# Kernel optimization log

Hardware: AMD Instinct MI355X
Metric: run time of the kernel (lower is better)

Reference implementation:

```python
import jax, jax.numpy as jnp
import numpy as np

B, T, U = 4, 256, 100
H_ENC, H_DEC = 512, 512
INPUT_SIZE = H_ENC + H_DEC  # 1024, joint='concat'
INNER = 512
VOCAB = 1024


def setup_inputs() -> dict:
    key = jax.random.key(0)
    k1, k2, k3, k4, k5, k6 = jax.random.split(key, 6)
    s_in = 1.0 / np.sqrt(INPUT_SIZE)
    s_h = 1.0 / np.sqrt(INNER)
    return {
        "enc_state": jax.random.normal(k1, (B, T, H_ENC), dtype=jnp.float32),
        "dec_state": jax.random.normal(k2, (B, U, H_DEC), dtype=jnp.float32),
        # mlp[0]: Linear(input_size -> inner): W1 [inner, input_size], b1 [inner]
        "W1": jax.random.uniform(k3, (INNER, INPUT_SIZE), jnp.float32, -s_in, s_in),
        "b1": jax.random.uniform(k4, (INNER,), jnp.float32, -s_in, s_in),
        # mlp[2]: Linear(inner -> vocab): W2 [vocab, inner], b2 [vocab]
        "W2": jax.random.uniform(k5, (VOCAB, INNER), jnp.float32, -s_h, s_h),
        "b2": jax.random.uniform(k6, (VOCAB,), jnp.float32, -s_h, s_h),
    }


def reference(enc_state, dec_state, W1, b1, W2, b2):
    # joint='concat': concat([enc broadcast over U, dec broadcast over T], -1)
    # then Linear -> tanh -> Linear.
    # Mathematically identical fused form: split W1 into enc/dec column blocks,
    # project each at native size, broadcast-add.
    h_enc = H_ENC
    W1e = W1[:, :h_enc]   # [inner, H_enc]
    W1d = W1[:, h_enc:]   # [inner, H_dec]
    pe = jnp.einsum('bth,ih->bti', enc_state, W1e)  # [B,T,inner]
    pd = jnp.einsum('buh,ih->bui', dec_state, W1d)  # [B,U,inner]
    hidden = jnp.tanh(pe[:, :, None, :] + pd[:, None, :, :] + b1)  # [B,T,U,inner]
    joint = jnp.einsum('btui,vi->btuv', hidden, W2) + b2  # [B,T,U,vocab]
    return joint
```

## Files before the change

kernel.cpp:

```cpp
#include <hip/hip_runtime.h>
#include <hip/hip_bf16.h>

#define NB 4
#define NT 256
#define NU 100
#define NH 512
#define NI 512
#define NV 1024
#define MROWS (NB * NT * NU)

typedef __attribute__((ext_vector_type(4))) float f32x4;
typedef __attribute__((ext_vector_type(8))) __bf16 bf16x8;

static __device__ __forceinline__ unsigned int f2bf(float f) {
  unsigned int u = __float_as_uint(f);
  return (u + 0x7FFFu + ((u >> 16) & 1u)) >> 16;
}

static __device__ __forceinline__ float fast_tanh(float x) {
  float e = __expf(2.f * x);
  return 1.f - 2.f * __builtin_amdgcn_rcpf(1.f + e);
}

static __device__ __forceinline__ unsigned int cvt_pk_bf16(float lo, float hi) {
  unsigned int r;
  asm("v_cvt_pk_bf16_f32 %0, %1, %2" : "=v"(r) : "v"(lo), "v"(hi));
  return r;
}

__global__ __launch_bounds__(256) void proj_kernel(
    const float* __restrict__ enc, const float* __restrict__ dec,
    const float* __restrict__ W1, float* __restrict__ pe, float* __restrict__ pd) {
  __shared__ float As[64][17];
  __shared__ float Bs[64][17];
  const int bx = blockIdx.x;
  const float* A;
  float* P;
  int Mrows, colOff, row0;
  if (bx < 16) { A = enc; P = pe; Mrows = NB * NT; colOff = 0;  row0 = bx * 64; }
  else         { A = dec; P = pd; Mrows = NB * NU; colOff = NH; row0 = (bx - 16) * 64; }
  const int col0 = blockIdx.y * 64;
  const int tx = threadIdx.x;
  const int tr = tx >> 4, tc = tx & 15;
  const int lr = tx >> 2, lc = (tx & 3) * 4;
  float acc[4][4] = {};
  for (int k0 = 0; k0 < NH; k0 += 16) {
    float4 av = make_float4(0.f, 0.f, 0.f, 0.f);
    if (row0 + lr < Mrows)
      av = *(const float4*)(A + (size_t)(row0 + lr) * NH + k0 + lc);
    float4 bv = *(const float4*)(W1 + (size_t)(col0 + lr) * (NH + NH) + colOff + k0 + lc);
    As[lr][lc] = av.x; As[lr][lc + 1] = av.y; As[lr][lc + 2] = av.z; As[lr][lc + 3] = av.w;
    Bs[lr][lc] = bv.x; Bs[lr][lc + 1] = bv.y; Bs[lr][lc + 2] = bv.z; Bs[lr][lc + 3] = bv.w;
    __syncthreads();
#pragma unroll
    for (int kk = 0; kk < 16; ++kk) {
      float a4[4], b4[4];
#pragma unroll
      for (int i = 0; i < 4; ++i) { a4[i] = As[tr * 4 + i][kk]; b4[i] = Bs[tc * 4 + i][kk]; }
#pragma unroll
      for (int i = 0; i < 4; ++i)
#pragma unroll
        for (int j = 0; j < 4; ++j) acc[i][j] = fmaf(a4[i], b4[j], acc[i][j]);
    }
    __syncthreads();
  }
#pragma unroll
  for (int i = 0; i < 4; ++i) {
    int r = row0 + tr * 4 + i;
    if (r < Mrows) {
#pragma unroll
      for (int j = 0; j < 4; ++j)
        P[(size_t)r * NI + col0 + tc * 4 + j] = acc[i][j];
    }
  }
}

__global__ __launch_bounds__(256) void cvt_w2_frag_kernel(
    const float* __restrict__ W2, unsigned short* __restrict__ w2f) {
  int g = blockIdx.x * 256 + threadIdx.x;
  int lr = g & 15, lq = (g >> 4) & 3;
  int cb = (g >> 6) & 15, kt = (g >> 10) & 15, nt = (g >> 14) & 3;
  int v = nt * 256 + cb * 16 + lr;
  int k = kt * 32 + lq * 8;
  const float* src = W2 + (size_t)v * NI + k;
  float4 a = *(const float4*)src;
  float4 b = *(const float4*)(src + 4);
  uint4 o;
  o.x = f2bf(a.x) | (f2bf(a.y) << 16);
  o.y = f2bf(a.z) | (f2bf(a.w) << 16);
  o.z = f2bf(b.x) | (f2bf(b.y) << 16);
  o.w = f2bf(b.z) | (f2bf(b.w) << 16);
  *(uint4*)(w2f + (size_t)g * 8) = o;
}

__global__ __launch_bounds__(512, 2) void fused_joint_kernel(
    const float* __restrict__ pe, const float* __restrict__ pd,
    const float* __restrict__ b1, const unsigned short* __restrict__ w2f,
    const float* __restrict__ b2, float* __restrict__ out) {
  __shared__ unsigned char ldsA[131072];
  const int tx = threadIdx.x;
  const int R0 = blockIdx.x * 128;
  const int lane = tx & 63, wid = tx >> 6;
  const int wr = wid >> 2, wc = wid & 3;
  const int lr = lane & 15, lq = lane >> 4;

  const unsigned short* w2base = w2f + ((size_t)(wc * 4) * 64 + lq * 16 + lr) * 8;
#define LOADB(DST, G) do {                                                    \
    const unsigned short* s_ = w2base + ((size_t)(G) << 13);                  \
    DST##0 = *(const bf16x8*)(s_);                                            \
    DST##1 = *(const bf16x8*)(s_ + 512);                                      \
    DST##2 = *(const bf16x8*)(s_ + 1024);                                     \
    DST##3 = *(const bf16x8*)(s_ + 1536);                                     \
  } while (0)

  bf16x8 bA0, bA1, bA2, bA3, bB0, bB1, bB2, bB3;
  LOADB(bA, 0);

#pragma unroll 2
  for (int pass = 0; pass < 16; ++pass) {
    int idx = pass * 512 + tx;
    int row = idx >> 6;
    int g8 = idx & 63;
    int i0 = g8 * 8;
    int grow = R0 + row;
    int b = grow / (NT * NU);
    int rem = grow - b * (NT * NU);
    int t = rem / NU;
    int u = rem - t * NU;
    const float* peP = pe + (size_t)(b * NT + t) * NI + i0;
    const float* pdP = pd + (size_t)(b * NU + u) * NI + i0;
    float4 p0 = *(const float4*)peP, p1 = *(const float4*)(peP + 4);
    float4 q0 = *(const float4*)pdP, q1 = *(const float4*)(pdP + 4);
    float4 c0 = *(const float4*)(b1 + i0), c1 = *(const float4*)(b1 + i0 + 4);
    uint4 pk;
    pk.x = cvt_pk_bf16(fast_tanh(p0.x + q0.x + c0.x), fast_tanh(p0.y + q0.y + c0.y));
    pk.y = cvt_pk_bf16(fast_tanh(p0.z + q0.z + c0.z), fast_tanh(p0.w + q0.w + c0.w));
    pk.z = cvt_pk_bf16(fast_tanh(p1.x + q1.x + c1.x), fast_tanh(p1.y + q1.y + c1.y));
    pk.w = cvt_pk_bf16(fast_tanh(p1.z + q1.z + c1.z), fast_tanh(p1.w + q1.w + c1.w));
    *(uint4*)(ldsA + row * 1024 + ((g8 ^ (row & 7)) << 4)) = pk;
  }
  __syncthreads();

  f32x4 acc[4][4];
#pragma unroll
  for (int mf = 0; mf < 4; ++mf)
#pragma unroll
    for (int nf = 0; nf < 4; ++nf)
#pragma unroll
      for (int z = 0; z < 4; ++z) acc[mf][nf][z] = 0.f;

#define COMPUTE(BV, G) do {                                                   \
    const int kt_ = (G) & 15;                                                 \
    bf16x8 af_[4];                                                            \
    _Pragma("unroll")                                                         \
    for (int mf = 0; mf < 4; ++mf) {                                          \
      int row_ = wr * 64 + mf * 16 + lr;                                      \
      af_[mf] = *(const bf16x8*)(ldsA + row_ * 1024 +                         \
                                 (((kt_ * 4 + lq) ^ (lr & 7)) << 4));         \
    }                                                                         \
    __builtin_amdgcn_s_setprio(1);                                            \
    _Pragma("unroll")                                                         \
    for (int mf = 0; mf < 4; ++mf) {                                          \
      acc[mf][0] = __builtin_amdgcn_mfma_f32_16x16x32_bf16(af_[mf], BV##0, acc[mf][0], 0, 0, 0); \
      acc[mf][1] = __builtin_amdgcn_mfma_f32_16x16x32_bf16(af_[mf], BV##1, acc[mf][1], 0, 0, 0); \
      acc[mf][2] = __builtin_amdgcn_mfma_f32_16x16x32_bf16(af_[mf], BV##2, acc[mf][2], 0, 0, 0); \
      acc[mf][3] = __builtin_amdgcn_mfma_f32_16x16x32_bf16(af_[mf], BV##3, acc[mf][3], 0, 0, 0); \
    }                                                                         \
    __builtin_amdgcn_s_setprio(0);                                            \
    if (kt_ == 15) {                                                          \
      const int np_ = (G) >> 4;                                               \
      _Pragma("unroll")                                                       \
      for (int nf = 0; nf < 4; ++nf) {                                        \
        int col_ = np_ * 256 + wc * 64 + nf * 16 + lr;                        \
        float bb_ = b2[col_];                                                 \
        _Pragma("unroll")                                                     \
        for (int mf = 0; mf < 4; ++mf) {                                      \
          _Pragma("unroll")                                                   \
          for (int j = 0; j < 4; ++j) {                                       \
            int grow_ = R0 + wr * 64 + mf * 16 + lq * 4 + j;                  \
            out[(size_t)grow_ * NV + col_] = acc[mf][nf][j] + bb_;            \
            acc[mf][nf][j] = 0.f;                                             \
          }                                                                   \
        }                                                                     \
      }                                                                       \
    }                                                                         \
  } while (0)

  for (int g = 0; g < 64; g += 2) {
    LOADB(bB, g + 1);
    COMPUTE(bA, g);
    if (g + 2 < 64) LOADB(bA, g + 2);
    COMPUTE(bB, g + 1);
  }
#undef COMPUTE
#undef LOADB
}

extern "C" void kernel_launch(void* const* d_in, const int* in_sizes, int n_in,
                              void* d_out, int out_size, void* d_ws, size_t ws_size,
                              hipStream_t stream) {
  const float* enc = (const float*)d_in[0];
  const float* dec = (const float*)d_in[1];
  const float* W1  = (const float*)d_in[2];
  const float* b1  = (const float*)d_in[3];
  const float* W2  = (const float*)d_in[4];
  const float* b2  = (const float*)d_in[5];
  float* out = (float*)d_out;
  char* ws = (char*)d_ws;

  float* pe = (float*)ws;
  float* pd = (float*)(ws + (2u << 20));
  unsigned short* w2f = (unsigned short*)(ws + (3u << 20));

  proj_kernel<<<dim3(23, 8), 256, 0, stream>>>(enc, dec, W1, pe, pd);
  cvt_w2_frag_kernel<<<256, 256, 0, stream>>>(W2, w2f);
  fused_joint_kernel<<<MROWS / 128, 512, 0, stream>>>(pe, pd, b1, w2f, b2, out);
}
```

Before: 228.6 us.

## Stage W2 tiles into double-buffered LDS via global_load_lds

The W2 operand was loaded straight from global memory into registers by each wave. It is now copied cooperatively into a double-buffered 32KB LDS region using the asynchronous global-to-LDS load instruction. Each wave then reads its B fragments from LDS, so the waves that share a column group no longer fetch duplicate global data, and VGPR pressure from the prefetch registers goes down. In exchange the loop adds a block-wide barrier on every k-step and extra LDS reads, and the block's LDS footprint grows to 160KB.

```diff
diff --git a/kernel.cpp b/kernel.cpp
--- a/kernel.cpp
+++ b/kernel.cpp
@@ -26,6 +26,12 @@
   unsigned int r;
   asm("v_cvt_pk_bf16_f32 %0, %1, %2" : "=v"(r) : "v"(lo), "v"(hi));
   return r;
+}
+
+static __device__ __forceinline__ void gload16(const void* g, void* l) {
+  __builtin_amdgcn_global_load_lds(
+      (const __attribute__((address_space(1))) unsigned int*)(g),
+      (__attribute__((address_space(3))) unsigned int*)(l), 16, 0, 0);
 }
 
 __global__ __launch_bounds__(256) void proj_kernel(
@@ -98,23 +104,21 @@
     const float* __restrict__ b1, const unsigned short* __restrict__ w2f,
     const float* __restrict__ b2, float* __restrict__ out) {
   __shared__ unsigned char ldsA[131072];
+  __shared__ unsigned char ldsB[32768];
   const int tx = threadIdx.x;
   const int R0 = blockIdx.x * 128;
   const int lane = tx & 63, wid = tx >> 6;
   const int wr = wid >> 2, wc = wid & 3;
   const int lr = lane & 15, lq = lane >> 4;
 
-  const unsigned short* w2base = w2f + ((size_t)(wc * 4) * 64 + lq * 16 + lr) * 8;
-#define LOADB(DST, G) do {                                                    \
-    const unsigned short* s_ = w2base + ((size_t)(G) << 13);                  \
-    DST##0 = *(const bf16x8*)(s_);                                            \
-    DST##1 = *(const bf16x8*)(s_ + 512);                                      \
-    DST##2 = *(const bf16x8*)(s_ + 1024);                                     \
-    DST##3 = *(const bf16x8*)(s_ + 1536);                                     \
+#define STAGEB(G, SLOT) do {                                                  \
+    unsigned char* dB_ = ldsB + (SLOT) * 16384;                               \
+    const unsigned char* src_ = (const unsigned char*)w2f + ((size_t)(G) << 14); \
+    gload16(src_ + tx * 16, dB_ + tx * 16);                                   \
+    gload16(src_ + (512 + tx) * 16, dB_ + (512 + tx) * 16);                   \
   } while (0)
 
-  bf16x8 bA0, bA1, bA2, bA3, bB0, bB1, bB2, bB3;
-  LOADB(bA, 0);
+  STAGEB(0, 0);
 
 #pragma unroll 2
   for (int pass = 0; pass < 16; ++pass) {
@@ -149,51 +153,50 @@
 #pragma unroll
       for (int z = 0; z < 4; ++z) acc[mf][nf][z] = 0.f;
 
-#define COMPUTE(BV, G) do {                                                   \
-    const int kt_ = (G) & 15;                                                 \
-    bf16x8 af_[4];                                                            \
-    _Pragma("unroll")                                                         \
-    for (int mf = 0; mf < 4; ++mf) {                                          \
-      int row_ = wr * 64 + mf * 16 + lr;                                      \
-      af_[mf] = *(const bf16x8*)(ldsA + row_ * 1024 +                         \
-                                 (((kt_ * 4 + lq) ^ (lr & 7)) << 4));         \
-    }                                                                         \
-    __builtin_amdgcn_s_setprio(1);                                            \
-    _Pragma("unroll")                                                         \
-    for (int mf = 0; mf < 4; ++mf) {                                          \
-      acc[mf][0] = __builtin_amdgcn_mfma_f32_16x16x32_bf16(af_[mf], BV##0, acc[mf][0], 0, 0, 0); \
-      acc[mf][1] = __builtin_amdgcn_mfma_f32_16x16x32_bf16(af_[mf], BV##1, acc[mf][1], 0, 0, 0); \
-      acc[mf][2] = __builtin_amdgcn_mfma_f32_16x16x32_bf16(af_[mf], BV##2, acc[mf][2], 0, 0, 0); \
-      acc[mf][3] = __builtin_amdgcn_mfma_f32_16x16x32_bf16(af_[mf], BV##3, acc[mf][3], 0, 0, 0); \
-    }                                                                         \
-    __builtin_amdgcn_s_setprio(0);                                            \
-    if (kt_ == 15) {                                                          \
-      const int np_ = (G) >> 4;                                               \
-      _Pragma("unroll")                                                       \
-      for (int nf = 0; nf < 4; ++nf) {                                        \
-        int col_ = np_ * 256 + wc * 64 + nf * 16 + lr;                        \
-        float bb_ = b2[col_];                                                 \
-        _Pragma("unroll")                                                     \
-        for (int mf = 0; mf < 4; ++mf) {                                      \
-          _Pragma("unroll")                                                   \
-          for (int j = 0; j < 4; ++j) {                                       \
-            int grow_ = R0 + wr * 64 + mf * 16 + lq * 4 + j;                  \
-            out[(size_t)grow_ * NV + col_] = acc[mf][nf][j] + bb_;            \
-            acc[mf][nf][j] = 0.f;                                             \
-          }                                                                   \
-        }                                                                     \
-      }                                                                       \
-    }                                                                         \
-  } while (0)
-
-  for (int g = 0; g < 64; g += 2) {
-    LOADB(bB, g + 1);
-    COMPUTE(bA, g);
-    if (g + 2 < 64) LOADB(bA, g + 2);
-    COMPUTE(bB, g + 1);
-  }
-#undef COMPUTE
-#undef LOADB
+  for (int g = 0; g < 64; ++g) {
+    const int kt = g & 15, slot = g & 1;
+    if (g < 63) STAGEB(g + 1, slot ^ 1);
+    const unsigned char* Bb = ldsB + slot * 16384;
+
+    bf16x8 af4[4], bfv[4];
+#pragma unroll
+    for (int nf = 0; nf < 4; ++nf)
+      bfv[nf] = *(const bf16x8*)(Bb + ((wc * 4 + nf) * 64 + lq * 16 + lr) * 16);
+#pragma unroll
+    for (int mf = 0; mf < 4; ++mf) {
+      int row = wr * 64 + mf * 16 + lr;
+      af4[mf] = *(const bf16x8*)(ldsA + row * 1024 +
+                                 (((kt * 4 + lq) ^ (row & 7)) << 4));
+    }
+    __builtin_amdgcn_s_setprio(1);
+#pragma unroll
+    for (int mf = 0; mf < 4; ++mf)
+#pragma unroll
+      for (int nf = 0; nf < 4; ++nf)
+        acc[mf][nf] = __builtin_amdgcn_mfma_f32_16x16x32_bf16(
+            af4[mf], bfv[nf], acc[mf][nf], 0, 0, 0);
+    __builtin_amdgcn_s_setprio(0);
+
+    if (kt == 15) {
+      const int np = g >> 4;
+#pragma unroll
+      for (int nf = 0; nf < 4; ++nf) {
+        int col = np * 256 + wc * 64 + nf * 16 + lr;
+        float bb = b2[col];
+#pragma unroll
+        for (int mf = 0; mf < 4; ++mf) {
+#pragma unroll
+          for (int j = 0; j < 4; ++j) {
+            int grow = R0 + wr * 64 + mf * 16 + lq * 4 + j;
+            out[(size_t)grow * NV + col] = acc[mf][nf][j] + bb;
+            acc[mf][nf][j] = 0.f;
+          }
+        }
+      }
+    }
+    if (g < 63) __syncthreads();
+  }
+#undef STAGEB
 }
 
 extern "C" void kernel_launch(void* const* d_in, const int* in_sizes, int n_in,
```

Measured after the change: 333.5 us. 45.9% more time.
